# Optimization experiments

Hardware: AMD Instinct MI355X
Metric: run time of the kernel (lower is better)

Reference implementation:

```python
import jax, jax.numpy as jnp
import numpy as np

J, F_ = 17, 32  # joints x per-joint features; C = J*F_ = 544
H = 8           # num_heads
EPS = 1e-5


def _layernorm(x, g, b):
    mu = jnp.mean(x, axis=-1, keepdims=True)
    var = jnp.mean((x - mu) ** 2, axis=-1, keepdims=True)
    return (x - mu) * jax.lax.rsqrt(var + EPS) * g + b


def setup_inputs() -> dict:
    key = jax.random.key(0)
    ks = jax.random.split(key, 8)
    B, N, C = 8, 1024, J * F_
    x = jax.random.normal(ks[0], (B, N, C), dtype=jnp.float32)
    s = 1.0 / np.sqrt(C)
    return {
        "x": x,
        "norm_g": jnp.ones((F_,), jnp.float32),
        "norm_b": jnp.zeros((F_,), jnp.float32),
        "ap_w": jax.random.normal(ks[1], (1, F_), jnp.float32) / np.sqrt(F_),
        "ap_b": jnp.zeros((1,), jnp.float32),
        "norm2_g": jnp.ones((C,), jnp.float32),
        "norm2_b": jnp.zeros((C,), jnp.float32),
        "qkv_w": jax.random.normal(ks[2], (3 * C, C), jnp.float32) * s,
        "proj_w": jax.random.normal(ks[3], (C, C), jnp.float32) * s,
        "proj_b": jnp.zeros((C,), jnp.float32),
        "scaling_factor": jnp.array([2.0], jnp.float32),
    }


def reference(x, norm_g, norm_b, ap_w, ap_b, norm2_g, norm2_b, qkv_w, proj_w, proj_b, scaling_factor):
    B, N, C = x.shape
    hd = C // H
    # --- attention pooling over joints ---
    xr = x.reshape(B, N, J, F_)
    xr = _layernorm(xr, norm_g, norm_b)                      # [B,N,17,32]
    scores = jnp.einsum('bnjf,of->bnjo', xr, ap_w)[..., 0] + ap_b[0]  # [B,N,17]
    # nn.Softmax(dim=1): softmax over sequence axis N (faithful to source)
    w = jax.nn.softmax(scores, axis=1)
    xp = (xr * w[..., None]).reshape(B, N, C)
    xp = _layernorm(xp, norm2_g, norm2_b)
    # --- position-scaled self-attention ---
    positions = jnp.linspace(0.0, 1.0, N, dtype=jnp.float32)  # [N]
    pos_scale = jnp.exp(-scaling_factor[0] * (positions - 0.5) ** 2)  # per-key scale
    qkv = (xp @ qkv_w.T).reshape(B, N, 3, H, hd)
    q = qkv[:, :, 0].transpose(0, 2, 1, 3)  # [B,H,N,hd]
    k = qkv[:, :, 1].transpose(0, 2, 1, 3)
    v = qkv[:, :, 2].transpose(0, 2, 1, 3)
    scale = hd ** -0.5
    attn = jnp.einsum('bhqd,bhkd->bhqk', q, k) * (scale * pos_scale[None, None, None, :])
    attn = jax.nn.softmax(attn, axis=-1)
    out = jnp.einsum('bhqk,bhkd->bhqd', attn, v)
    out = out.transpose(0, 2, 1, 3).reshape(B, N, C)
    return out @ proj_w.T + proj_b
```

## Files before the change

### kernel.cpp

```cpp
#include <hip/hip_runtime.h>
#include <hip/hip_bf16.h>

#define BB 8
#define NN 1024
#define CC 544
#define JJ 17
#define FF 32
#define HH 8
#define HD 68
#define BN 8192
#define KD 544
#define NCQ 1632
#define NCQP 1664
#define NCPP 640
#define NKB 9
#define BHSZ 73728
#define AQR 64

using f32x4  = __attribute__((ext_vector_type(4))) float;
using bf16x8 = __attribute__((ext_vector_type(8))) short;

__device__ __forceinline__ void gld_lds16(const void* g, void* l) {
  __builtin_amdgcn_global_load_lds(
      (const __attribute__((address_space(1))) void*)g,
      (__attribute__((address_space(3))) void*)l, 16, 0, 0);
}

__global__ __launch_bounds__(256) void wconv(const float* __restrict__ qkv_w,
                                             const float* __restrict__ proj_w,
                                             __hip_bfloat16* __restrict__ qw,
                                             __hip_bfloat16* __restrict__ pw,
                                             char* __restrict__ qkp) {
  int bid = blockIdx.x, t = threadIdx.x;
  if (bid < NCQP + NCPP) {
    bool isq = bid < NCQP;
    int r = isq ? bid : bid - NCQP;
    const float* src = isq ? qkv_w : proj_w;
    __hip_bfloat16* dst = isq ? qw : pw;
    int nrows = isq ? NCQ : CC;
    if (t < KD / 4) {
      int c = t * 4;
      float4 v;
      if (r < nrows) v = *(const float4*)(src + (size_t)r * KD + c);
      else           v = float4{0.f, 0.f, 0.f, 0.f};
      __hip_bfloat16 o[4] = {__float2bfloat16(v.x), __float2bfloat16(v.y),
                             __float2bfloat16(v.z), __float2bfloat16(v.w)};
      *(unsigned long long*)(dst + (size_t)r * KD + c) = *(unsigned long long*)o;
    }
  } else {
    int row = (bid - (NCQP + NCPP)) * 256 + t;
    if (row < 131072) {
      int bhT = row >> 10, n = row & 1023;
      char* p = qkp + (size_t)bhT * 147456 + 131072 + (size_t)n * 16 + 8;
      *(unsigned long long*)p = 0ull;
    }
  }
}

__global__ __launch_bounds__(256) void ln1_scores(const float* __restrict__ x,
                                                  const float* __restrict__ g,
                                                  const float* __restrict__ bta,
                                                  const float* __restrict__ apw,
                                                  const float* __restrict__ apb,
                                                  __hip_bfloat16* __restrict__ xr,
                                                  float* __restrict__ scores) {
  int wv = threadIdx.x >> 6, lane = threadIdx.x & 63;
  int bn = blockIdx.x * 4 + wv;
  int f = lane & 31, half = lane >> 5;
  const float* row = x + (size_t)bn * CC;
  float gg = g[f], bb = bta[f], aw = apw[f], ab = apb[0];
  for (int it = 0; it < 9; ++it) {
    int j = it * 2 + half;
    bool act = (j < JJ);
    float v = act ? row[j * FF + f] : 0.f;
    float s = v;
    for (int m = 16; m >= 1; m >>= 1) s += __shfl_xor(s, m);
    float mu = s * (1.f / 32.f);
    float dv = v - mu;
    float s2 = dv * dv;
    for (int m = 16; m >= 1; m >>= 1) s2 += __shfl_xor(s2, m);
    float xn = dv * rsqrtf(s2 * (1.f / 32.f) + 1e-5f) * gg + bb;
    float sc = xn * aw;
    for (int m = 16; m >= 1; m >>= 1) sc += __shfl_xor(sc, m);
    if (act) {
      xr[(size_t)bn * CC + j * FF + f] = __float2bfloat16(xn);
      if (f == 0) scores[bn * JJ + j] = sc + ab;
    }
  }
}

__global__ __launch_bounds__(256) void softmax_red(const float* __restrict__ scores,
                                                   float2* __restrict__ tab) {
  int bj = blockIdx.x;
  int b = bj / JJ, j = bj - b * JJ;
  const float* s = scores + (size_t)b * NN * JJ + j;
  int t = threadIdx.x;
  float v[4];
  float mx = -1e30f;
#pragma unroll
  for (int i = 0; i < 4; ++i) { v[i] = s[(t + 256 * i) * JJ]; mx = fmaxf(mx, v[i]); }
#pragma unroll
  for (int m = 32; m >= 1; m >>= 1) mx = fmaxf(mx, __shfl_xor(mx, m));
  __shared__ float red[4];
  if ((t & 63) == 0) red[t >> 6] = mx;
  __syncthreads();
  mx = fmaxf(fmaxf(red[0], red[1]), fmaxf(red[2], red[3]));
  float sum = 0.f;
#pragma unroll
  for (int i = 0; i < 4; ++i) sum += __expf(v[i] - mx);
#pragma unroll
  for (int m = 32; m >= 1; m >>= 1) sum += __shfl_xor(sum, m);
  __shared__ float red2[4];
  if ((t & 63) == 0) red2[t >> 6] = sum;
  __syncthreads();
  if (t == 0) {
    sum = red2[0] + red2[1] + red2[2] + red2[3];
    tab[bj] = make_float2(mx, 1.f / sum);
  }
}

__global__ __launch_bounds__(256) void ln2_xp(const __hip_bfloat16* __restrict__ xr,
                                              const float* __restrict__ scores,
                                              const float2* __restrict__ tab,
                                              const float* __restrict__ g2,
                                              const float* __restrict__ b2,
                                              __hip_bfloat16* __restrict__ xp) {
  __shared__ float wsh[4][JJ];
  int wv = threadIdx.x >> 6, lane = threadIdx.x & 63;
  int bn = blockIdx.x * 4 + wv;
  if (lane < JJ) {
    float sc = scores[bn * JJ + lane];
    float2 mi = tab[(bn >> 10) * JJ + lane];
    wsh[wv][lane] = __expf(sc - mi.x) * mi.y;
  }
  float vals[9];
  float sum = 0.f;
  for (int it = 0; it < 9; ++it) {
    int c = it * 64 + lane;
    float v = 0.f;
    if (c < CC) v = __bfloat162float(xr[(size_t)bn * CC + c]) * wsh[wv][c >> 5];
    vals[it] = v;
    sum += v;
  }
  for (int m = 32; m >= 1; m >>= 1) sum += __shfl_xor(sum, m);
  float mu = sum * (1.f / 544.f);
  float s2 = 0.f;
  for (int it = 0; it < 9; ++it) {
    int c = it * 64 + lane;
    if (c < CC) { float dv = vals[it] - mu; s2 += dv * dv; }
  }
  for (int m = 32; m >= 1; m >>= 1) s2 += __shfl_xor(s2, m);
  float rstd = rsqrtf(s2 * (1.f / 544.f) + 1e-5f);
  for (int it = 0; it < 9; ++it) {
    int c = it * 64 + lane;
    if (c < CC)
      xp[(size_t)bn * CC + c] = __float2bfloat16((vals[it] - mu) * rstd * g2[c] + b2[c]);
  }
}

template <int MODE>
__global__ __launch_bounds__(256) void gemm_nt(const __hip_bfloat16* __restrict__ A,
                                               const __hip_bfloat16* __restrict__ Bw,
                                               __hip_bfloat16* __restrict__ Qp,
                                               __hip_bfloat16* __restrict__ Kp,
                                               __hip_bfloat16* __restrict__ Vt,
                                               float* __restrict__ Cf,
                                               const float* __restrict__ bias,
                                               const float* __restrict__ sfp) {
  extern __shared__ char smem[];
  __hip_bfloat16 (*As)[128 * 32] = (__hip_bfloat16 (*)[128 * 32])(smem);
  __hip_bfloat16 (*Bs)[128 * 32] = (__hip_bfloat16 (*)[128 * 32])(smem + 16384);
  const int t = threadIdx.x;
  const int w = t >> 6, lane = t & 63;
  const int fr = lane & 15, fq = lane >> 4;
  const int bi = blockIdx.x;
  const int xcd = bi & 7, j = bi >> 3;
  const int bx = xcd * 8 + (j & 7), by = j >> 3;
  const int m0 = bx * 128;
  const int n0 = by * 128;
  const int wm = (w >> 1) * 64, wn = (w & 1) * 64;

  f32x4 acc[4][4] = {};

  const __hip_bfloat16* Ag = A + (size_t)m0 * KD;
  const __hip_bfloat16* Bg = Bw + (size_t)n0 * KD;

#pragma unroll
  for (int i2 = 0; i2 < 2; ++i2) {
    int cb = (i2 * 4 + w) * 64;
    int chunk = cb + lane;
    int row = chunk >> 2, c16 = chunk & 3;
    gld_lds16(Ag + (size_t)row * KD + c16 * 8, &As[0][cb * 8]);
    gld_lds16(Bg + (size_t)row * KD + c16 * 8, &Bs[0][cb * 8]);
  }
  __syncthreads();

  for (int kt = 0; kt < 17; ++kt) {
    const int cur = kt & 1;
    if (kt < 16) {
      const int k0 = (kt + 1) * 32;
#pragma unroll
      for (int i2 = 0; i2 < 2; ++i2) {
        int cb = (i2 * 4 + w) * 64;
        int chunk = cb + lane;
        int row = chunk >> 2, c16 = chunk & 3;
        gld_lds16(Ag + (size_t)row * KD + k0 + c16 * 8, &As[1 - cur][cb * 8]);
        gld_lds16(Bg + (size_t)row * KD + k0 + c16 * 8, &Bs[1 - cur][cb * 8]);
      }
    }
    bf16x8 af[4], bfr[4];
#pragma unroll
    for (int tm = 0; tm < 4; ++tm)
      af[tm] = *(const bf16x8*)&As[cur][(wm + tm * 16 + fr) * 32 + fq * 8];
#pragma unroll
    for (int tn = 0; tn < 4; ++tn)
      bfr[tn] = *(const bf16x8*)&Bs[cur][(wn + tn * 16 + fr) * 32 + fq * 8];
#pragma unroll
    for (int tm = 0; tm < 4; ++tm)
#pragma unroll
      for (int tn = 0; tn < 4; ++tn)
        acc[tm][tn] = __builtin_amdgcn_mfma_f32_16x16x32_bf16(af[tm], bfr[tn], acc[tm][tn], 0, 0, 0);
    __syncthreads();
  }

  if (MODE == 1) {
#pragma unroll
    for (int tn = 0; tn < 4; ++tn) {
      int o = n0 + wn + tn * 16 + fr;
      if (o < CC) {
        float bb = bias[o];
#pragma unroll
        for (int tm = 0; tm < 4; ++tm) {
          int m = m0 + wm + tm * 16 + fq * 4;
#pragma unroll
          for (int r = 0; r < 4; ++r)
            Cf[(size_t)(m + r) * CC + o] = acc[tm][tn][r] + bb;
        }
      }
    }
  } else {
    const int b = m0 >> 10;
    const int nbase = m0 & (NN - 1);
    const float sf = sfp[0];
    __hip_bfloat16* Cst = (__hip_bfloat16*)smem;

#pragma unroll
    for (int tn = 0; tn < 4; ++tn) {
      int olocal = wn + tn * 16 + fr;
      int o = n0 + olocal;
      bool isk = (o >= CC) && (o < 2 * CC);
#pragma unroll
      for (int tm = 0; tm < 4; ++tm) {
        int mloc = wm + tm * 16 + fq * 4;
        int n = nbase + mloc;
#pragma unroll
        for (int r = 0; r < 4; ++r) {
          float v = acc[tm][tn][r];
          if (isk) {
            float pos = (n + r) * (1.f / 1023.f) - 0.5f;
            v *= __expf(-sf * pos * pos) * (0.12126781251816650f * 1.44269504088896340f);
          }
          Cst[olocal * 136 + mloc + r] = __float2bfloat16(v);
        }
      }
    }
    __syncthreads();

    for (int s = t; s < 32 * 128; s += 256) {
      int g = s >> 7, nl = s & 127;
      int o = n0 + g * 4;
      if (o < 2 * CC) {
        bool isk = o >= CC;
        int oo = isk ? o - CC : o;
        int h = oo / HD;
        int d0 = oo - h * HD;
        unsigned long long pk;
        __hip_bfloat16* pp = (__hip_bfloat16*)&pk;
#pragma unroll
        for (int j2 = 0; j2 < 4; ++j2) pp[j2] = Cst[(g * 4 + j2) * 136 + nl];
        __hip_bfloat16* basep = isk ? Kp : Qp;
        size_t ei = (size_t)(b * HH + h) * BHSZ + (size_t)(d0 >> 3) * (NN * 8) +
                    (size_t)(nbase + nl) * 8 + (d0 & 7);
        *(unsigned long long*)(basep + ei) = pk;
      }
    }
    {
      int lo = 2 * CC - n0; if (lo < 0) lo = 0;
      int hi = NCQ - n0;    if (hi > 128) hi = 128;
      if (hi > lo) {
        int nv = hi - lo;
        for (int s = t; s < nv * 16; s += 256) {
          int row = lo + (s >> 4), seg = s & 15;
          int oo = n0 + row - 2 * CC;
          int h = oo / HD;
          int d = oo - h * HD;
          bf16x8 v8 = *(const bf16x8*)&Cst[row * 136 + seg * 8];
          __hip_bfloat16* vdst = Vt + ((size_t)(b * HH + h) * HD + d) * NN + nbase + seg * 8;
          *(bf16x8*)vdst = v8;
        }
      }
    }
  }
}

__global__ __launch_bounds__(128) void attn_kernel(const __hip_bfloat16* __restrict__ Qp,
                                                   const __hip_bfloat16* __restrict__ Kp,
                                                   const __hip_bfloat16* __restrict__ Vt,
                                                   __hip_bfloat16* __restrict__ Ao) {
  __shared__ __hip_bfloat16 Qs[NKB * 64 * 8];
  __shared__ __hip_bfloat16 Ks[2][NKB * 64 * 8];
  __shared__ __hip_bfloat16 Zs[64 * 8];
  const int t = threadIdx.x;
  const int w = t >> 6, lane = t & 63;
  const int fr = lane & 15, fq = lane >> 4;
  const int idx = blockIdx.x;
  const int bh = idx & 63, qt = idx >> 6;
  const int h = bh & 7, b = bh >> 3;

  const __hip_bfloat16* qtile = Qp + (size_t)bh * BHSZ + (size_t)qt * AQR * 8;
  const __hip_bfloat16* kbase = Kp + (size_t)bh * BHSZ;
  const __hip_bfloat16* vbase = Vt + (size_t)bh * HD * NN;

  *(unsigned long long*)&Zs[t * 4] = 0ull;
#pragma unroll
  for (int i = 0; i < 5; ++i) {
    int kb = i * 2 + w;
    if (kb < NKB) gld_lds16(qtile + (size_t)kb * (NN * 8) + lane * 8, &Qs[kb * 64 * 8]);
  }
#pragma unroll
  for (int i = 0; i < 5; ++i) {
    int kb = i * 2 + w;
    if (kb < NKB) gld_lds16(kbase + (size_t)kb * (NN * 8) + lane * 8, &Ks[0][kb * 64 * 8]);
  }
  __syncthreads();
  bf16x8 qa[2][3];
#pragma unroll
  for (int ks = 0; ks < 3; ++ks) {
    const __hip_bfloat16* qb = (ks < 2 || fq == 0) ? &Qs[(ks * 4 + fq) * 512] : Zs;
#pragma unroll
    for (int g = 0; g < 2; ++g)
      qa[g][ks] = *(const bf16x8*)&qb[(w * 32 + g * 16 + fr) * 8];
  }
  __syncthreads();

  f32x4 o_acc[2][5] = {};
  float l_part[2][4] = {};
  const int dclamp = (fr < 4) ? 0 : 1;

  for (int kt = 0; kt < 16; ++kt) {
    const int cur = kt & 1;
    bf16x8 vfrag[5][2];
#pragma unroll
    for (int tv = 0; tv < 5; ++tv) {
      int d = tv * 16 + fr;
      int dc = (tv == 4 && dclamp) ? 0 : d;
#pragma unroll
      for (int ks2 = 0; ks2 < 2; ++ks2)
        vfrag[tv][ks2] = *(const bf16x8*)(vbase + (size_t)dc * NN + kt * 64 + ks2 * 32 + fq * 8);
    }
    if (kt < 15) {
      const __hip_bfloat16* ktile = kbase + (size_t)(kt + 1) * 64 * 8;
#pragma unroll
      for (int i = 0; i < 5; ++i) {
        int kb = i * 2 + w;
        if (kb < NKB) gld_lds16(ktile + (size_t)kb * (NN * 8) + lane * 8, &Ks[1 - cur][kb * 64 * 8]);
      }
    }

    f32x4 s[2][4] = {};
#pragma unroll
    for (int ks = 0; ks < 3; ++ks) {
      const __hip_bfloat16* kbL = (ks < 2 || fq == 0) ? &Ks[cur][(ks * 4 + fq) * 512] : Zs;
#pragma unroll
      for (int tn = 0; tn < 4; ++tn) {
        bf16x8 kb = *(const bf16x8*)&kbL[(tn * 16 + fr) * 8];
        s[0][tn] = __builtin_amdgcn_mfma_f32_16x16x32_bf16(qa[0][ks], kb, s[0][tn], 0, 0, 0);
        s[1][tn] = __builtin_amdgcn_mfma_f32_16x16x32_bf16(qa[1][ks], kb, s[1][tn], 0, 0, 0);
      }
    }
#pragma unroll
    for (int g = 0; g < 2; ++g) {
      __hip_bfloat16* Pw = &Qs[(w * 2 + g) * 1152];
#pragma unroll
      for (int tn = 0; tn < 4; ++tn)
#pragma unroll
        for (int r = 0; r < 4; ++r) {
          float pe = __builtin_amdgcn_exp2f(s[g][tn][r]);
          l_part[g][r] += pe;
          Pw[(fq * 4 + r) * 72 + tn * 16 + fr] = __float2bfloat16(pe);
        }
    }
#pragma unroll
    for (int ks2 = 0; ks2 < 2; ++ks2) {
      bf16x8 pa0 = *(const bf16x8*)&Qs[(w * 2 + 0) * 1152 + fr * 72 + ks2 * 32 + fq * 8];
      bf16x8 pa1 = *(const bf16x8*)&Qs[(w * 2 + 1) * 1152 + fr * 72 + ks2 * 32 + fq * 8];
#pragma unroll
      for (int tv = 0; tv < 5; ++tv) {
        o_acc[0][tv] = __builtin_amdgcn_mfma_f32_16x16x32_bf16(pa0, vfrag[tv][ks2], o_acc[0][tv], 0, 0, 0);
        o_acc[1][tv] = __builtin_amdgcn_mfma_f32_16x16x32_bf16(pa1, vfrag[tv][ks2], o_acc[1][tv], 0, 0, 0);
      }
    }
    __syncthreads();
  }
#pragma unroll
  for (int g = 0; g < 2; ++g) {
    __hip_bfloat16* obase = Ao + (size_t)(b * NN + qt * AQR + w * 32 + g * 16) * CC + h * HD;
    float inv[4];
#pragma unroll
    for (int r = 0; r < 4; ++r) {
      float l = l_part[g][r];
#pragma unroll
      for (int msk = 8; msk >= 1; msk >>= 1) l += __shfl_xor(l, msk);
      inv[r] = 1.f / l;
    }
#pragma unroll
    for (int tv = 0; tv < 5; ++tv) {
      int d = tv * 16 + fr;
      if (d < HD) {
#pragma unroll
        for (int r = 0; r < 4; ++r)
          obase[(size_t)(fq * 4 + r) * CC + d] = __float2bfloat16(o_acc[g][tv][r] * inv[r]);
      }
    }
  }
}

extern "C" void kernel_launch(void* const* d_in, const int* in_sizes, int n_in,
                              void* d_out, int out_size, void* d_ws, size_t ws_size,
                              hipStream_t stream) {
  (void)in_sizes; (void)n_in; (void)out_size; (void)ws_size;
  const float* x       = (const float*)d_in[0];
  const float* norm_g  = (const float*)d_in[1];
  const float* norm_b  = (const float*)d_in[2];
  const float* ap_w    = (const float*)d_in[3];
  const float* ap_b    = (const float*)d_in[4];
  const float* norm2_g = (const float*)d_in[5];
  const float* norm2_b = (const float*)d_in[6];
  const float* qkv_w   = (const float*)d_in[7];
  const float* proj_w  = (const float*)d_in[8];
  const float* proj_b  = (const float*)d_in[9];
  const float* sf      = (const float*)d_in[10];
  float* out = (float*)d_out;
  char* ws = (char*)d_ws;

  __hip_bfloat16* xr   = (__hip_bfloat16*)(ws);
  float* scores        = (float*)(ws + 8912896);
  float2* tab          = (float2*)(ws + 9469952);
  __hip_bfloat16* xp   = (__hip_bfloat16*)(ws + 9474048);
  __hip_bfloat16* qw   = (__hip_bfloat16*)(ws + 18386944);
  __hip_bfloat16* pw   = (__hip_bfloat16*)(ws + 20197376);
  __hip_bfloat16* vt   = (__hip_bfloat16*)(ws + 20893696);
  __hip_bfloat16* ao   = (__hip_bfloat16*)(ws + 29806592);
  __hip_bfloat16* qp   = (__hip_bfloat16*)(ws + 38719488);
  __hip_bfloat16* kp   = (__hip_bfloat16*)(ws + 48156672);

  wconv<<<NCQP + NCPP + 512, 256, 0, stream>>>(qkv_w, proj_w, qw, pw, (char*)qp);
  ln1_scores<<<BN / 4, 256, 0, stream>>>(x, norm_g, norm_b, ap_w, ap_b, xr, scores);
  softmax_red<<<BB * JJ, 256, 0, stream>>>(scores, tab);
  ln2_xp<<<BN / 4, 256, 0, stream>>>(xr, scores, tab, norm2_g, norm2_b, xp);
  gemm_nt<0><<<dim3(64 * 13), 256, 34816, stream>>>(xp, qw, qp, kp, vt, nullptr, nullptr, sf);
  attn_kernel<<<dim3((NN / AQR) * HH * BB), 128, 0, stream>>>(qp, kp, vt, ao);
  gemm_nt<1><<<dim3(64 * 5), 256, 34816, stream>>>(ao, pw, nullptr, nullptr, nullptr, out, proj_b, nullptr);
}
```

Before: 200.9 us.

## Load Q and K fragments directly into registers, drop LDS staging and block barriers

The attention kernel no longer stages Q and double-buffered K tiles through shared memory with async global-to-LDS loads and per-tile __syncthreads. Each wave now loads its Q fragments and the K fragments for the next tile straight from global memory into registers, ping-ponging between two register sets. Shared memory is kept only for the per-wave P tile. The intent is to remove barrier stalls and LDS traffic and to shrink LDS use. In exchange register pressure rises (hence launch_bounds(128,1)), and the same K data is now fetched redundantly by each wave.

```diff
diff --git a/kernel.cpp b/kernel.cpp
--- a/kernel.cpp
+++ b/kernel.cpp
@@ -303,13 +303,11 @@
   }
 }
 
-__global__ __launch_bounds__(128) void attn_kernel(const __hip_bfloat16* __restrict__ Qp,
-                                                   const __hip_bfloat16* __restrict__ Kp,
-                                                   const __hip_bfloat16* __restrict__ Vt,
-                                                   __hip_bfloat16* __restrict__ Ao) {
-  __shared__ __hip_bfloat16 Qs[NKB * 64 * 8];
-  __shared__ __hip_bfloat16 Ks[2][NKB * 64 * 8];
-  __shared__ __hip_bfloat16 Zs[64 * 8];
+__global__ __launch_bounds__(128, 1) void attn_kernel(const __hip_bfloat16* __restrict__ Qp,
+                                                      const __hip_bfloat16* __restrict__ Kp,
+                                                      const __hip_bfloat16* __restrict__ Vt,
+                                                      __hip_bfloat16* __restrict__ Ao) {
+  __shared__ __hip_bfloat16 Ps[4 * 1152];
   const int t = threadIdx.x;
   const int w = t >> 6, lane = t & 63;
   const int fr = lane & 15, fq = lane >> 4;
@@ -317,91 +315,91 @@
   const int bh = idx & 63, qt = idx >> 6;
   const int h = bh & 7, b = bh >> 3;
 
-  const __hip_bfloat16* qtile = Qp + (size_t)bh * BHSZ + (size_t)qt * AQR * 8;
+  const __hip_bfloat16* qbase = Qp + (size_t)bh * BHSZ;
   const __hip_bfloat16* kbase = Kp + (size_t)bh * BHSZ;
   const __hip_bfloat16* vbase = Vt + (size_t)bh * HD * NN;
 
-  *(unsigned long long*)&Zs[t * 4] = 0ull;
-#pragma unroll
-  for (int i = 0; i < 5; ++i) {
-    int kb = i * 2 + w;
-    if (kb < NKB) gld_lds16(qtile + (size_t)kb * (NN * 8) + lane * 8, &Qs[kb * 64 * 8]);
-  }
-#pragma unroll
-  for (int i = 0; i < 5; ++i) {
-    int kb = i * 2 + w;
-    if (kb < NKB) gld_lds16(kbase + (size_t)kb * (NN * 8) + lane * 8, &Ks[0][kb * 64 * 8]);
-  }
-  __syncthreads();
+  const bf16x8 zero8 = {};
+
   bf16x8 qa[2][3];
 #pragma unroll
   for (int ks = 0; ks < 3; ++ks) {
-    const __hip_bfloat16* qb = (ks < 2 || fq == 0) ? &Qs[(ks * 4 + fq) * 512] : Zs;
-#pragma unroll
-    for (int g = 0; g < 2; ++g)
-      qa[g][ks] = *(const bf16x8*)&qb[(w * 32 + g * 16 + fr) * 8];
-  }
-  __syncthreads();
+    int kblk = ks * 4 + fq;
+    int kbc = kblk > 8 ? 8 : kblk;
+#pragma unroll
+    for (int g = 0; g < 2; ++g) {
+      bf16x8 v = *(const bf16x8*)(qbase + (size_t)kbc * (NN * 8) +
+                                  ((size_t)qt * AQR + w * 32 + g * 16 + fr) * 8);
+      if (kblk > 8) v = zero8;
+      qa[g][ks] = v;
+    }
+  }
 
   f32x4 o_acc[2][5] = {};
   float l_part[2][4] = {};
   const int dclamp = (fr < 4) ? 0 : 1;
 
-  for (int kt = 0; kt < 16; ++kt) {
-    const int cur = kt & 1;
-    bf16x8 vfrag[5][2];
-#pragma unroll
-    for (int tv = 0; tv < 5; ++tv) {
-      int d = tv * 16 + fr;
-      int dc = (tv == 4 && dclamp) ? 0 : d;
-#pragma unroll
-      for (int ks2 = 0; ks2 < 2; ++ks2)
-        vfrag[tv][ks2] = *(const bf16x8*)(vbase + (size_t)dc * NN + kt * 64 + ks2 * 32 + fq * 8);
-    }
-    if (kt < 15) {
-      const __hip_bfloat16* ktile = kbase + (size_t)(kt + 1) * 64 * 8;
-#pragma unroll
-      for (int i = 0; i < 5; ++i) {
-        int kb = i * 2 + w;
-        if (kb < NKB) gld_lds16(ktile + (size_t)kb * (NN * 8) + lane * 8, &Ks[1 - cur][kb * 64 * 8]);
-      }
-    }
-
-    f32x4 s[2][4] = {};
-#pragma unroll
-    for (int ks = 0; ks < 3; ++ks) {
-      const __hip_bfloat16* kbL = (ks < 2 || fq == 0) ? &Ks[cur][(ks * 4 + fq) * 512] : Zs;
-#pragma unroll
-      for (int tn = 0; tn < 4; ++tn) {
-        bf16x8 kb = *(const bf16x8*)&kbL[(tn * 16 + fr) * 8];
-        s[0][tn] = __builtin_amdgcn_mfma_f32_16x16x32_bf16(qa[0][ks], kb, s[0][tn], 0, 0, 0);
-        s[1][tn] = __builtin_amdgcn_mfma_f32_16x16x32_bf16(qa[1][ks], kb, s[1][tn], 0, 0, 0);
-      }
-    }
-#pragma unroll
-    for (int g = 0; g < 2; ++g) {
-      __hip_bfloat16* Pw = &Qs[(w * 2 + g) * 1152];
-#pragma unroll
-      for (int tn = 0; tn < 4; ++tn)
-#pragma unroll
-        for (int r = 0; r < 4; ++r) {
-          float pe = __builtin_amdgcn_exp2f(s[g][tn][r]);
-          l_part[g][r] += pe;
-          Pw[(fq * 4 + r) * 72 + tn * 16 + fr] = __float2bfloat16(pe);
-        }
-    }
-#pragma unroll
-    for (int ks2 = 0; ks2 < 2; ++ks2) {
-      bf16x8 pa0 = *(const bf16x8*)&Qs[(w * 2 + 0) * 1152 + fr * 72 + ks2 * 32 + fq * 8];
-      bf16x8 pa1 = *(const bf16x8*)&Qs[(w * 2 + 1) * 1152 + fr * 72 + ks2 * 32 + fq * 8];
-#pragma unroll
-      for (int tv = 0; tv < 5; ++tv) {
-        o_acc[0][tv] = __builtin_amdgcn_mfma_f32_16x16x32_bf16(pa0, vfrag[tv][ks2], o_acc[0][tv], 0, 0, 0);
-        o_acc[1][tv] = __builtin_amdgcn_mfma_f32_16x16x32_bf16(pa1, vfrag[tv][ks2], o_acc[1][tv], 0, 0, 0);
-      }
-    }
-    __syncthreads();
-  }
+#define LDK(KN, KTN)                                                                   \
+  {                                                                                    \
+    _Pragma("unroll") for (int ks = 0; ks < 3; ++ks) {                                 \
+      int kblk = ks * 4 + fq;                                                          \
+      int kbc = kblk > 8 ? 8 : kblk;                                                   \
+      const __hip_bfloat16* kp0 =                                                      \
+          kbase + (size_t)kbc * (NN * 8) + ((size_t)(KTN) * 64 + fr) * 8;              \
+      _Pragma("unroll") for (int tn = 0; tn < 4; ++tn) {                               \
+        bf16x8 v = *(const bf16x8*)(kp0 + tn * 128);                                   \
+        if (kblk > 8) v = zero8;                                                       \
+        KN[ks][tn] = v;                                                                \
+      }                                                                                \
+    }                                                                                  \
+  }
+
+#define PHASE(KC, KN, KT)                                                              \
+  {                                                                                    \
+    bf16x8 vfrag[5][2];                                                                \
+    _Pragma("unroll") for (int tv = 0; tv < 5; ++tv) {                                 \
+      int d = tv * 16 + fr;                                                            \
+      int dc = (tv == 4 && dclamp) ? 0 : d;                                            \
+      _Pragma("unroll") for (int ks2 = 0; ks2 < 2; ++ks2)                              \
+          vfrag[tv][ks2] =                                                             \
+          *(const bf16x8*)(vbase + (size_t)dc * NN + (KT) * 64 + ks2 * 32 + fq * 8);   \
+    }                                                                                  \
+    LDK(KN, ((KT) + 1) & 15);                                                          \
+    _Pragma("unroll") for (int g = 0; g < 2; ++g) {                                    \
+      f32x4 s[4] = {};                                                                 \
+      _Pragma("unroll") for (int ks = 0; ks < 3; ++ks)                                 \
+          _Pragma("unroll") for (int tn = 0; tn < 4; ++tn)                             \
+              s[tn] = __builtin_amdgcn_mfma_f32_16x16x32_bf16(qa[g][ks], KC[ks][tn],   \
+                                                              s[tn], 0, 0, 0);         \
+      __hip_bfloat16* Pw = &Ps[(w * 2 + g) * 1152];                                    \
+      _Pragma("unroll") for (int tn = 0; tn < 4; ++tn)                                 \
+          _Pragma("unroll") for (int r = 0; r < 4; ++r) {                              \
+        float pe = __builtin_amdgcn_exp2f(s[tn][r]);                                   \
+        l_part[g][r] += pe;                                                            \
+        Pw[(fq * 4 + r) * 72 + tn * 16 + fr] = __float2bfloat16(pe);                   \
+      }                                                                                \
+    }                                                                                  \
+    _Pragma("unroll") for (int ks2 = 0; ks2 < 2; ++ks2) {                              \
+      bf16x8 pa0 = *(const bf16x8*)&Ps[(w * 2 + 0) * 1152 + fr * 72 + ks2 * 32 + fq * 8]; \
+      bf16x8 pa1 = *(const bf16x8*)&Ps[(w * 2 + 1) * 1152 + fr * 72 + ks2 * 32 + fq * 8]; \
+      _Pragma("unroll") for (int tv = 0; tv < 5; ++tv) {                               \
+        o_acc[0][tv] = __builtin_amdgcn_mfma_f32_16x16x32_bf16(pa0, vfrag[tv][ks2],    \
+                                                               o_acc[0][tv], 0, 0, 0); \
+        o_acc[1][tv] = __builtin_amdgcn_mfma_f32_16x16x32_bf16(pa1, vfrag[tv][ks2],    \
+                                                               o_acc[1][tv], 0, 0, 0); \
+      }                                                                                \
+    }                                                                                  \
+  }
+
+  bf16x8 kfA[3][4], kfB[3][4];
+  LDK(kfA, 0);
+  for (int kt = 0; kt < 16; kt += 2) {
+    PHASE(kfA, kfB, kt);
+    PHASE(kfB, kfA, kt + 1);
+  }
+#undef PHASE
+#undef LDK
+
 #pragma unroll
   for (int g = 0; g < 2; ++g) {
     __hip_bfloat16* obase = Ao + (size_t)(b * NN + qt * AQR + w * 32 + g * 16) * CC + h * HD;
```

Measured after the change: 222.9 us. 1.11x slower.
